# Performance work log

Hardware: AMD Instinct MI355X
Metric: run time of the kernel (lower is better)

The kernel has to match this reference:

```python
import jax, jax.numpy as jnp
import numpy as np

E = 512   # embed_dim
H = 16    # num_heads
D = E // H  # head_dim = 32
L = 2048  # target (query) length
S = 2048  # source (stored pattern) length
N = 4     # batch
LN_EPS = 1e-5


def setup_inputs() -> dict:
    key = jax.random.key(0)
    ks = jax.random.split(key, 8)
    inv_sqrt_e = 1.0 / np.sqrt(E).astype(np.float32)
    return {
        "query": jax.random.normal(ks[0], (L, N, E), jnp.float32),
        "key_in": jax.random.normal(ks[1], (S, N, E), jnp.float32),
        "value": jax.random.normal(ks[2], (S, N, E), jnp.float32),
        "scaling": jax.random.uniform(ks[3], (H,), jnp.float32),  # per-head beta
        "in_proj_weight": jax.random.normal(ks[4], (3 * E, E), jnp.float32) * inv_sqrt_e,
        "in_proj_bias": jnp.zeros((3 * E,), jnp.float32),
        "p_norm_weight": jnp.ones((D,), jnp.float32),
        "p_norm_bias": jnp.zeros((D,), jnp.float32),
        "out_proj_weight": jax.random.normal(ks[5], (E, E), jnp.float32) * inv_sqrt_e,
        "out_proj_bias": jnp.zeros((E,), jnp.float32),
    }


def reference(query, key_in, value, scaling, in_proj_weight, in_proj_bias,
              p_norm_weight, p_norm_bias, out_proj_weight, out_proj_bias):
    Lq, Nb, Ed = query.shape
    Sk = key_in.shape[0]
    # split packed in-projection (torch Linear convention: y = x @ W^T + b)
    wq, wk, wv = jnp.split(in_proj_weight, 3, axis=0)
    bq, bk, bv = jnp.split(in_proj_bias, 3, axis=0)
    q = jnp.einsum('lne,fe->lnf', query, wq) + bq
    k = jnp.einsum('sne,fe->snf', key_in, wk) + bk
    v = jnp.einsum('sne,fe->snf', value, wv) + bv
    # (len, N, H*D) -> (N, H, len, D)
    q = q.reshape(Lq, Nb, H, D).transpose(1, 2, 0, 3)
    k = k.reshape(Sk, Nb, H, D).transpose(1, 2, 0, 3)
    v = v.reshape(Sk, Nb, H, D).transpose(1, 2, 0, 3)

    def pattern_norm(x):
        # affine LayerNorm over the association (head) dimension D
        mu = jnp.mean(x, axis=-1, keepdims=True)
        var = jnp.mean(jnp.square(x - mu), axis=-1, keepdims=True)
        return (x - mu) * jax.lax.rsqrt(var + LN_EPS) * p_norm_weight + p_norm_bias

    k = pattern_norm(k)
    v = pattern_norm(v)

    beta = scaling.reshape(1, H, 1, 1)  # per-head inverse-temperature
    scores = jnp.einsum('nhld,nhsd->nhls', q * beta, k)  # [N,H,L,S]
    attn = jax.nn.softmax(scores, axis=-1)  # single Hopfield update (update_steps_max=0)
    out = jnp.einsum('nhls,nhsd->nhld', attn, v)  # [N,H,L,D]
    out = out.transpose(2, 0, 1, 3).reshape(Lq, Nb, H * D)
    out = jnp.einsum('lnf,of->lno', out, out_proj_weight) + out_proj_bias
    return out  # (L, N, E)
```

## Files before the change

kernel.cpp:

```cpp
#include <hip/hip_runtime.h>
#include <cstdint>

#define LN_EPS 1e-5f

typedef _Float16 f16;
typedef _Float16 half4_t __attribute__((ext_vector_type(4)));
typedef _Float16 half8_t __attribute__((ext_vector_type(8)));
typedef __fp16 fp16v2 __attribute__((ext_vector_type(2)));
typedef float f32x4 __attribute__((ext_vector_type(4)));

__device__ __forceinline__ void gl_lds16(const void* g, void* l) {
    __builtin_amdgcn_global_load_lds(
        (__attribute__((address_space(1))) void*)(uintptr_t)g,
        (__attribute__((address_space(3))) void*)(uint32_t)(uintptr_t)l,
        16, 0, 0);
}

__device__ __forceinline__ half4_t pack4(float a, float b, float c, float d) {
    fp16v2 lo = __builtin_amdgcn_cvt_pkrtz(a, b);
    fp16v2 hi = __builtin_amdgcn_cvt_pkrtz(c, d);
    half4_t r;
    r[0] = (f16)lo[0]; r[1] = (f16)lo[1]; r[2] = (f16)hi[0]; r[3] = (f16)hi[1];
    return r;
}

__global__ void k_cast(const float* __restrict__ W1f, const float* __restrict__ W2f,
                       const float* __restrict__ Xq, const float* __restrict__ Xk,
                       const float* __restrict__ Xv,
                       f16* __restrict__ W1h, f16* __restrict__ W2h,
                       f16* __restrict__ Xh) {
    int t = blockIdx.x * blockDim.x + threadIdx.x;
    const float4* src;
    half4_t* dst;
    int idx;
    if (t < 196608)      { src = (const float4*)W1f; dst = (half4_t*)W1h; idx = t; }
    else if (t < 262144) { src = (const float4*)W2f; dst = (half4_t*)W2h; idx = t - 196608; }
    else {
        int u = t - 262144;
        int s = u >> 20;
        idx = u & 1048575;
        src = (s == 0) ? (const float4*)Xq : ((s == 1) ? (const float4*)Xk : (const float4*)Xv);
        dst = (half4_t*)(Xh + (size_t)s * 4194304);
    }
    float4 v = src[idx];
    dst[idx] = pack4(v.x, v.y, v.z, v.w);
}

__global__ __launch_bounds__(256) void k_inproj(
    const f16* __restrict__ Xh, const f16* __restrict__ W1,
    const float* __restrict__ bias, const float* __restrict__ scaling,
    f16* __restrict__ Qg, f16* __restrict__ Kg, f16* __restrict__ Vg)
{
    __shared__ __align__(16) f16 Al[3][128 * 32];
    __shared__ __align__(16) f16 Bl[3][128 * 32];

    const int tid = threadIdx.x;
    const int m0 = blockIdx.x * 128;
    const int f0 = blockIdx.y * 128;
    const int sec = f0 >> 9;
    const f16* X = Xh + (size_t)sec * 4194304;
    f16* Ob = (sec == 0) ? Qg : ((sec == 1) ? Kg : Vg);

    const int wid = tid >> 6, ln = tid & 63, l15 = ln & 15, quad = ln >> 4;
    const int wm = wid >> 1, wn = wid & 1;
    const int srow = ln >> 2, sco = (ln & 3) * 8;

    f32x4 z4 = {0.f, 0.f, 0.f, 0.f};
    f32x4 acc[4][4];
    #pragma unroll
    for (int i = 0; i < 4; ++i)
        #pragma unroll
        for (int j = 0; j < 4; ++j) acc[i][j] = z4;

    auto issue = [&](int kt, int slot) {
        const int k0 = kt * 32;
        #pragma unroll
        for (int i = 0; i < 2; ++i) {
            int row = wid * 32 + i * 16 + srow;
            gl_lds16(W1 + (size_t)(f0 + row) * 512 + k0 + sco,
                     Bl[slot] + (wid * 32 + i * 16) * 32);
            gl_lds16(X + (size_t)(m0 + row) * 512 + k0 + sco,
                     Al[slot] + (wid * 32 + i * 16) * 32);
        }
    };
    issue(0, 0);
    issue(1, 1);

    int slot = 0;
    for (int kt = 0; kt < 16; ++kt) {
        if (kt < 15) asm volatile("s_waitcnt vmcnt(4)" ::: "memory");
        else         asm volatile("s_waitcnt vmcnt(0)" ::: "memory");
        __builtin_amdgcn_s_barrier();

        if (kt < 14) {
            int nb = slot + 2; if (nb >= 3) nb -= 3;
            issue(kt + 2, nb);
        }

        half8_t a[4], b[4];
        #pragma unroll
        for (int i = 0; i < 4; ++i)
            a[i] = *(const half8_t*)(Al[slot] + (wm * 64 + i * 16 + l15) * 32 + quad * 8);
        #pragma unroll
        for (int j = 0; j < 4; ++j)
            b[j] = *(const half8_t*)(Bl[slot] + (wn * 64 + j * 16 + l15) * 32 + quad * 8);
        __builtin_amdgcn_s_setprio(1);
        #pragma unroll
        for (int i = 0; i < 4; ++i)
            #pragma unroll
            for (int j = 0; j < 4; ++j)
                acc[i][j] = __builtin_amdgcn_mfma_f32_16x16x32_f16(b[j], a[i], acc[i][j], 0, 0, 0);
        __builtin_amdgcn_s_setprio(0);

        slot = slot + 1; if (slot == 3) slot = 0;
    }

    #pragma unroll
    for (int j = 0; j < 4; ++j) {
        int fb = f0 + wn * 64 + j * 16;
        int floc = (fb & 511) + quad * 4;
        int hh = floc >> 5;
        int cc = (floc >> 3) & 3, e0 = floc & 7;
        float sc2 = (sec == 0) ? scaling[hh] * 1.44269504f : 1.0f;
        float4 bs4 = *(const float4*)(bias + fb + quad * 4);
        #pragma unroll
        for (int i = 0; i < 4; ++i) {
            int rm = m0 + wm * 64 + i * 16 + l15;
            int l = rm >> 2, nb = rm & 3;
            int gg = nb * 16 + hh;
            *(half4_t*)(Ob + (size_t)gg * 65536 + (size_t)cc * 16384 + (size_t)l * 8 + e0) =
                pack4((acc[i][j][0] + bs4.x) * sc2, (acc[i][j][1] + bs4.y) * sc2,
                      (acc[i][j][2] + bs4.z) * sc2, (acc[i][j][3] + bs4.w) * sc2);
        }
    }
}

__global__ void k_norm_kv(f16* __restrict__ Kg, const f16* __restrict__ Vg,
                          const float* __restrict__ w, const float* __restrict__ b,
                          f16* __restrict__ Vtg) {
    __shared__ __align__(16) f16 T[32 * 64];
    const int t = threadIdx.x;
    const int seg = blockIdx.x, g = blockIdx.y;
    const int s_l = t >> 2, c = t & 3;
    const size_t base = (size_t)g * 65536 + (size_t)c * 16384 + (size_t)(seg * 64 + s_l) * 8;

    half8_t kv = *(const half8_t*)(Kg + base);
    half8_t vv = *(const half8_t*)(Vg + base);
    float kf[8], vf[8];
    float ks1 = 0.f, ks2 = 0.f, vs1 = 0.f, vs2 = 0.f;
    #pragma unroll
    for (int j = 0; j < 8; ++j) {
        kf[j] = (float)kv[j]; ks1 += kf[j]; ks2 += kf[j] * kf[j];
        vf[j] = (float)vv[j]; vs1 += vf[j]; vs2 += vf[j] * vf[j];
    }
    ks1 += __shfl_xor(ks1, 1); ks1 += __shfl_xor(ks1, 2);
    ks2 += __shfl_xor(ks2, 1); ks2 += __shfl_xor(ks2, 2);
    vs1 += __shfl_xor(vs1, 1); vs1 += __shfl_xor(vs1, 2);
    vs2 += __shfl_xor(vs2, 1); vs2 += __shfl_xor(vs2, 2);
    float kmu = ks1 * (1.f / 32.f), kvar = ks2 * (1.f / 32.f) - kmu * kmu;
    float vmu = vs1 * (1.f / 32.f), vvar = vs2 * (1.f / 32.f) - vmu * vmu;
    float krs = rsqrtf(kvar + LN_EPS), vrs = rsqrtf(vvar + LN_EPS);

    half8_t ky;
    int cs = s_l >> 3, es = s_l & 7;
    #pragma unroll
    for (int j = 0; j < 8; ++j) {
        int d = c * 8 + j;
        float wd = w[d], bd = b[d];
        ky[j] = (f16)((kf[j] - kmu) * krs * wd + bd);
        T[d * 64 + (cs ^ j) * 8 + es] = (f16)((vf[j] - vmu) * vrs * wd + bd);
    }
    *(half8_t*)(Kg + base) = ky;
    __syncthreads();
    int d_o = t >> 3, c_o = t & 7;
    half8_t out = *(const half8_t*)(T + d_o * 64 + c_o * 8);
    *(half8_t*)(Vtg + (size_t)(g * 32 + seg) * 2048 + d_o * 64 + c_o * 8) = out;
}

__global__ __launch_bounds__(256, 4) void k_flash(
    const f16* __restrict__ Qg, const f16* __restrict__ Kg,
    const f16* __restrict__ Vtg, f16* __restrict__ Og)
{
    __shared__ __align__(16) char smem[40960];

    const int tid = threadIdx.x, wid = tid >> 6, ln = tid & 63;
    const int l15 = ln & 15, quad = ln >> 4, l8 = ln & 7;
    char* Pw = smem + 24576 + wid * 4096;
    const int g = blockIdx.x, h = g & 15, n = g >> 4;
    const int q0 = blockIdx.y * 128;

    half8_t aq[2];
    #pragma unroll
    for (int i = 0; i < 2; ++i)
        aq[i] = *(const half8_t*)(Qg + (size_t)g * 65536 + (size_t)quad * 16384 +
                                  (size_t)(q0 + wid * 32 + i * 16 + l15) * 8);

    const f16* kp = Kg + (size_t)g * 65536 + (size_t)wid * 16384;
    const f16* vp = Vtg + (size_t)(g * 32) * 2048 + wid * 512;
    gl_lds16(kp + (size_t)ln * 8, smem + wid * 1024);
    gl_lds16(vp + (size_t)ln * 8, smem + 12288 + wid * 1024);
    gl_lds16(kp + 512 + (size_t)ln * 8, smem + 4096 + wid * 1024);
    gl_lds16(vp + 2048 + (size_t)ln * 8, smem + 12288 + 4096 + wid * 1024);
    kp += 1024;
    vp += 4096;

    half8_t onesf;
    {
        f16 o = (l15 == 0) ? (f16)1.0f : (f16)0.0f;
        #pragma unroll
        for (int j = 0; j < 8; ++j) onesf[j] = o;
    }

    f32x4 z4 = {0.f, 0.f, 0.f, 0.f};
    f32x4 accO[2][2], accSum[2];
    accO[0][0] = z4; accO[0][1] = z4; accO[1][0] = z4; accO[1][1] = z4;
    accSum[0] = z4; accSum[1] = z4;
    float m_i[2] = {-1e30f, -1e30f};

    int cur = 0;
    for (int st = 0; st < 32; ++st) {
        if (st < 31) asm volatile("s_waitcnt vmcnt(2)" ::: "memory");
        else         asm volatile("s_waitcnt vmcnt(0)" ::: "memory");
        __builtin_amdgcn_s_barrier();

        if (st < 30) {
            int nb = cur + 2; if (nb >= 3) nb -= 3;
            gl_lds16(kp + (size_t)ln * 8, smem + nb * 4096 + wid * 1024);
            gl_lds16(vp + (size_t)ln * 8, smem + 12288 + nb * 4096 + wid * 1024);
            kp += 512;
            vp += 2048;
        }
        const char* Kl = smem + cur * 4096;
        const char* Vt = smem + 12288 + cur * 4096;

        half8_t ak[4];
        #pragma unroll
        for (int mt = 0; mt < 4; ++mt)
            ak[mt] = *(const half8_t*)(Kl + quad * 1024 + (mt * 16 + l15) * 16);
        f32x4 accS[2][4];
        __builtin_amdgcn_s_setprio(1);
        #pragma unroll
        for (int i = 0; i < 2; ++i)
            #pragma unroll
            for (int mt = 0; mt < 4; ++mt)
                accS[i][mt] = __builtin_amdgcn_mfma_f32_16x16x32_f16(ak[mt], aq[i], z4, 0, 0, 0);
        __builtin_amdgcn_s_setprio(0);

        float mn[2];
        bool up = false;
        #pragma unroll
        for (int i = 0; i < 2; ++i) {
            float xm = fmaxf(fmaxf(accS[i][0][0], accS[i][0][1]),
                             fmaxf(accS[i][0][2], accS[i][0][3]));
            #pragma unroll
            for (int mt = 1; mt < 4; ++mt)
                xm = fmaxf(xm, fmaxf(fmaxf(accS[i][mt][0], accS[i][mt][1]),
                                     fmaxf(accS[i][mt][2], accS[i][mt][3])));
            xm = fmaxf(xm, __shfl_xor(xm, 16));
            xm = fmaxf(xm, __shfl_xor(xm, 32));
            up = up || (xm > m_i[i] + 8.f);
            mn[i] = fmaxf(m_i[i], xm);
        }
        if (__ballot(up)) {
            #pragma unroll
            for (int i = 0; i < 2; ++i) {
                float alpha = __builtin_amdgcn_exp2f(m_i[i] - mn[i]);
                #pragma unroll
                for (int dt = 0; dt < 2; ++dt)
                    #pragma unroll
                    for (int r = 0; r < 4; ++r) accO[i][dt][r] *= alpha;
                #pragma unroll
                for (int r = 0; r < 4; ++r) accSum[i][r] *= alpha;
                m_i[i] = mn[i];
            }
        }

        #pragma unroll
        for (int i = 0; i < 2; ++i) {
            #pragma unroll
            for (int mt = 0; mt < 4; ++mt) {
                float p0 = __builtin_amdgcn_exp2f(accS[i][mt][0] - m_i[i]);
                float p1 = __builtin_amdgcn_exp2f(accS[i][mt][1] - m_i[i]);
                float p2 = __builtin_amdgcn_exp2f(accS[i][mt][2] - m_i[i]);
                float p3 = __builtin_amdgcn_exp2f(accS[i][mt][3] - m_i[i]);
                int ch = (mt * 2 + (quad >> 1)) ^ l8;
                *(half4_t*)(Pw + (i * 16 + l15) * 128 + ch * 16 + (quad & 1) * 8) =
                    pack4(p0, p1, p2, p3);
            }
        }

        #pragma unroll
        for (int kt = 0; kt < 2; ++kt) {
            half8_t av[2], bp[2];
            #pragma unroll
            for (int dt = 0; dt < 2; ++dt) {
                int d = dt * 16 + l15;
                int cp = (kt * 4 + quad) ^ (l15 & 7);
                av[dt] = *(const half8_t*)(Vt + d * 128 + cp * 16);
            }
            #pragma unroll
            for (int i = 0; i < 2; ++i)
                bp[i] = *(const half8_t*)(Pw + (i * 16 + l15) * 128 +
                                          (((kt * 4 + quad) ^ l8) * 16));
            __builtin_amdgcn_s_setprio(1);
            #pragma unroll
            for (int i = 0; i < 2; ++i) {
                #pragma unroll
                for (int dt = 0; dt < 2; ++dt)
                    accO[i][dt] = __builtin_amdgcn_mfma_f32_16x16x32_f16(av[dt], bp[i], accO[i][dt], 0, 0, 0);
                accSum[i] = __builtin_amdgcn_mfma_f32_16x16x32_f16(onesf, bp[i], accSum[i], 0, 0, 0);
            }
            __builtin_amdgcn_s_setprio(0);
        }

        cur = cur + 1; if (cur == 3) cur = 0;
    }

    #pragma unroll
    for (int i = 0; i < 2; ++i) {
        float li = __shfl(accSum[i][0], l15);
        float inv = 1.f / li;
        #pragma unroll
        for (int dt = 0; dt < 2; ++dt)
            *(half4_t*)(Pw + (i * 16 + l15) * 80 + (dt * 16 + quad * 4) * 2) =
                pack4(accO[i][dt][0] * inv, accO[i][dt][1] * inv,
                      accO[i][dt][2] * inv, accO[i][dt][3] * inv);
    }
    int q2 = ln >> 1, hf = ln & 1;
    half8_t o0 = *(const half8_t*)(Pw + q2 * 80 + hf * 32);
    half8_t o1 = *(const half8_t*)(Pw + q2 * 80 + hf * 32 + 16);
    size_t rowe = ((size_t)(n * 2048 + q0 + wid * 32 + q2)) * 512 + h * 32 + hf * 16;
    *(half8_t*)(Og + rowe) = o0;
    *(half8_t*)(Og + rowe + 8) = o1;
}

__global__ __launch_bounds__(256) void k_outproj(
    const f16* __restrict__ A, const f16* __restrict__ W2,
    const float* __restrict__ bias, float* __restrict__ Out)
{
    __shared__ __align__(16) f16 Al[3][64 * 32];
    __shared__ __align__(16) f16 Bl[3][128 * 32];

    const int tid = threadIdx.x;
    const int m0 = blockIdx.x * 64;
    const int f0 = blockIdx.y * 128;
    const int wid = tid >> 6, ln = tid & 63, l15 = ln & 15, quad = ln >> 4;
    const int wm = wid >> 1, wn = wid & 1;
    const int srow = ln >> 2, sco = (ln & 3) * 8;

    f32x4 z4 = {0.f, 0.f, 0.f, 0.f};
    f32x4 acc[2][4];
    #pragma unroll
    for (int i = 0; i < 2; ++i)
        #pragma unroll
        for (int j = 0; j < 4; ++j) acc[i][j] = z4;

    auto issue = [&](int kt, int slot) {
        const int k0 = kt * 32;
        int arow = wid * 16 + srow;
        gl_lds16(A + (size_t)(m0 + arow) * 512 + k0 + sco,
                 Al[slot] + wid * 512);
        #pragma unroll
        for (int i = 0; i < 2; ++i) {
            int brow = wid * 32 + i * 16 + srow;
            gl_lds16(W2 + (size_t)(f0 + brow) * 512 + k0 + sco,
                     Bl[slot] + (wid * 32 + i * 16) * 32);
        }
    };
    issue(0, 0);
    issue(1, 1);

    int slot = 0;
    for (int kt = 0; kt < 16; ++kt) {
        if (kt < 15) asm volatile("s_waitcnt vmcnt(3)" ::: "memory");
        else         asm volatile("s_waitcnt vmcnt(0)" ::: "memory");
        __builtin_amdgcn_s_barrier();

        if (kt < 14) {
            int nb = slot + 2; if (nb >= 3) nb -= 3;
            issue(kt + 2, nb);
        }

        half8_t a[2], b[4];
        #pragma unroll
        for (int i = 0; i < 2; ++i)
            a[i] = *(const half8_t*)(Al[slot] + (wm * 32 + i * 16 + l15) * 32 + quad * 8);
        #pragma unroll
        for (int j = 0; j < 4; ++j)
            b[j] = *(const half8_t*)(Bl[slot] + (wn * 64 + j * 16 + l15) * 32 + quad * 8);
        __builtin_amdgcn_s_setprio(1);
        #pragma unroll
        for (int i = 0; i < 2; ++i)
            #pragma unroll
            for (int j = 0; j < 4; ++j)
                acc[i][j] = __builtin_amdgcn_mfma_f32_16x16x32_f16(b[j], a[i], acc[i][j], 0, 0, 0);
        __builtin_amdgcn_s_setprio(0);

        slot = slot + 1; if (slot == 3) slot = 0;
    }

    #pragma unroll
    for (int j = 0; j < 4; ++j) {
        int fb = f0 + wn * 64 + j * 16;
        float4 bs4 = *(const float4*)(bias + fb + quad * 4);
        #pragma unroll
        for (int i = 0; i < 2; ++i) {
            int rm = m0 + wm * 32 + i * 16 + l15;
            int orow = (rm & 2047) * 4 + (rm >> 11);
            float4 o;
            o.x = acc[i][j][0] + bs4.x;
            o.y = acc[i][j][1] + bs4.y;
            o.z = acc[i][j][2] + bs4.z;
            o.w = acc[i][j][3] + bs4.w;
            *(float4*)(Out + (size_t)orow * 512 + fb + quad * 4) = o;
        }
    }
}

extern "C" void kernel_launch(void* const* d_in, const int* in_sizes, int n_in,
                              void* d_out, int out_size, void* d_ws, size_t ws_size,
                              hipStream_t stream) {
    const float* query   = (const float*)d_in[0];
    const float* key_in  = (const float*)d_in[1];
    const float* value   = (const float*)d_in[2];
    const float* scaling = (const float*)d_in[3];
    const float* ipw     = (const float*)d_in[4];
    const float* ipb     = (const float*)d_in[5];
    const float* pnw     = (const float*)d_in[6];
    const float* pnb     = (const float*)d_in[7];
    const float* opw     = (const float*)d_in[8];
    const float* opb     = (const float*)d_in[9];
    float* out = (float*)d_out;

    f16* Qg  = (f16*)d_ws;
    f16* Kg  = Qg + (size_t)4194304;
    f16* Vg  = Qg + (size_t)8388608;
    f16* W1  = Qg + (size_t)12582912;
    f16* W2  = Qg + (size_t)13369344;
    f16* Xh  = Qg + (size_t)13631488;
    f16* Vtg = Xh;
    f16* Og  = Vg;

    k_cast<<<13312, 256, 0, stream>>>(ipw, opw, query, key_in, value, W1, W2, Xh);
    k_inproj<<<dim3(64, 12), 256, 0, stream>>>(Xh, W1, ipb, scaling, Qg, Kg, Vg);
    k_norm_kv<<<dim3(32, 64), 256, 0, stream>>>(Kg, Vg, pnw, pnb, Vtg);
    k_flash<<<dim3(64, 16), 256, 0, stream>>>(Qg, Kg, Vtg, Og);
    k_outproj<<<dim3(128, 4), 256, 0, stream>>>(Og, W2, opb, out);
}
```

Measured before the change: 213.0 us.

## Stage GEMM epilogues through LDS for coalesced stores; grid-stride cast kernel

The in-projection and out-projection epilogues now write their accumulator tiles into a reused shared-memory pool, using an XOR swizzle in the in-projection, before streaming them to global memory in wide contiguous chunks. The previous direct stores were scattered 8-byte or row-strided 16-byte writes. The cast kernel now runs a quarter of the blocks, each thread converting four elements. The extra LDS round trip and barriers add latency in exchange for better write coalescing.

```diff
diff --git a/kernel.cpp b/kernel.cpp
--- a/kernel.cpp
+++ b/kernel.cpp
@@ -29,21 +29,25 @@
                        const float* __restrict__ Xv,
                        f16* __restrict__ W1h, f16* __restrict__ W2h,
                        f16* __restrict__ Xh) {
-    int t = blockIdx.x * blockDim.x + threadIdx.x;
-    const float4* src;
-    half4_t* dst;
-    int idx;
-    if (t < 196608)      { src = (const float4*)W1f; dst = (half4_t*)W1h; idx = t; }
-    else if (t < 262144) { src = (const float4*)W2f; dst = (half4_t*)W2h; idx = t - 196608; }
-    else {
-        int u = t - 262144;
-        int s = u >> 20;
-        idx = u & 1048575;
-        src = (s == 0) ? (const float4*)Xq : ((s == 1) ? (const float4*)Xk : (const float4*)Xv);
-        dst = (half4_t*)(Xh + (size_t)s * 4194304);
-    }
-    float4 v = src[idx];
-    dst[idx] = pack4(v.x, v.y, v.z, v.w);
+    int t0 = blockIdx.x * blockDim.x + threadIdx.x;
+    #pragma unroll
+    for (int rep = 0; rep < 4; ++rep) {
+        int t = t0 + rep * 851968;
+        const float4* src;
+        half4_t* dst;
+        int idx;
+        if (t < 196608)      { src = (const float4*)W1f; dst = (half4_t*)W1h; idx = t; }
+        else if (t < 262144) { src = (const float4*)W2f; dst = (half4_t*)W2h; idx = t - 196608; }
+        else {
+            int u = t - 262144;
+            int s = u >> 20;
+            idx = u & 1048575;
+            src = (s == 0) ? (const float4*)Xq : ((s == 1) ? (const float4*)Xk : (const float4*)Xv);
+            dst = (half4_t*)(Xh + (size_t)s * 4194304);
+        }
+        float4 v = src[idx];
+        dst[idx] = pack4(v.x, v.y, v.z, v.w);
+    }
 }
 
 __global__ __launch_bounds__(256) void k_inproj(
@@ -51,8 +55,7 @@
     const float* __restrict__ bias, const float* __restrict__ scaling,
     f16* __restrict__ Qg, f16* __restrict__ Kg, f16* __restrict__ Vg)
 {
-    __shared__ __align__(16) f16 Al[3][128 * 32];
-    __shared__ __align__(16) f16 Bl[3][128 * 32];
+    __shared__ __align__(16) char pool[49152];
 
     const int tid = threadIdx.x;
     const int m0 = blockIdx.x * 128;
@@ -74,13 +77,15 @@
 
     auto issue = [&](int kt, int slot) {
         const int k0 = kt * 32;
+        f16* As = (f16*)(pool + slot * 16384);
+        f16* Bs = (f16*)(pool + slot * 16384 + 8192);
         #pragma unroll
         for (int i = 0; i < 2; ++i) {
             int row = wid * 32 + i * 16 + srow;
             gl_lds16(W1 + (size_t)(f0 + row) * 512 + k0 + sco,
-                     Bl[slot] + (wid * 32 + i * 16) * 32);
+                     Bs + (wid * 32 + i * 16) * 32);
             gl_lds16(X + (size_t)(m0 + row) * 512 + k0 + sco,
-                     Al[slot] + (wid * 32 + i * 16) * 32);
+                     As + (wid * 32 + i * 16) * 32);
         }
     };
     issue(0, 0);
@@ -97,13 +102,15 @@
             issue(kt + 2, nb);
         }
 
+        const f16* As = (const f16*)(pool + slot * 16384);
+        const f16* Bs = (const f16*)(pool + slot * 16384 + 8192);
         half8_t a[4], b[4];
         #pragma unroll
         for (int i = 0; i < 4; ++i)
-            a[i] = *(const half8_t*)(Al[slot] + (wm * 64 + i * 16 + l15) * 32 + quad * 8);
+            a[i] = *(const half8_t*)(As + (wm * 64 + i * 16 + l15) * 32 + quad * 8);
         #pragma unroll
         for (int j = 0; j < 4; ++j)
-            b[j] = *(const half8_t*)(Bl[slot] + (wn * 64 + j * 16 + l15) * 32 + quad * 8);
+            b[j] = *(const half8_t*)(Bs + (wn * 64 + j * 16 + l15) * 32 + quad * 8);
         __builtin_amdgcn_s_setprio(1);
         #pragma unroll
         for (int i = 0; i < 4; ++i)
@@ -115,22 +122,40 @@
         slot = slot + 1; if (slot == 3) slot = 0;
     }
 
+    __syncthreads();
+    f16* Ep = (f16*)pool;
+
     #pragma unroll
     for (int j = 0; j < 4; ++j) {
-        int fb = f0 + wn * 64 + j * 16;
-        int floc = (fb & 511) + quad * 4;
-        int hh = floc >> 5;
-        int cc = (floc >> 3) & 3, e0 = floc & 7;
+        int floc0 = wn * 64 + j * 16 + quad * 4;
+        int fb = f0 + floc0;
+        int hh = (fb & 511) >> 5;
         float sc2 = (sec == 0) ? scaling[hh] * 1.44269504f : 1.0f;
-        float4 bs4 = *(const float4*)(bias + fb + quad * 4);
+        float4 bs4 = *(const float4*)(bias + fb);
         #pragma unroll
         for (int i = 0; i < 4; ++i) {
-            int rm = m0 + wm * 64 + i * 16 + l15;
-            int l = rm >> 2, nb = rm & 3;
-            int gg = nb * 16 + hh;
-            *(half4_t*)(Ob + (size_t)gg * 65536 + (size_t)cc * 16384 + (size_t)l * 8 + e0) =
+            int mloc = wm * 64 + i * 16 + l15;
+            int key = (mloc >> 2) & 7;
+            *(half4_t*)(Ep + mloc * 128 + (floc0 ^ (key << 3))) =
                 pack4((acc[i][j][0] + bs4.x) * sc2, (acc[i][j][1] + bs4.y) * sc2,
                       (acc[i][j][2] + bs4.z) * sc2, (acc[i][j][3] + bs4.w) * sc2);
+        }
+    }
+    __syncthreads();
+
+    {
+        int fgrp = (tid >> 6) * 4 + quad;
+        int fs = (f0 & 511) + fgrp * 8;
+        int hh = fs >> 5, cc = (fs >> 3) & 3;
+        #pragma unroll
+        for (int it = 0; it < 8; ++it) {
+            int nb = it & 3, lblk = it >> 2;
+            int L = lblk * 16 + l15;
+            int mloc = nb + 4 * L;
+            half8_t v = *(const half8_t*)(Ep + mloc * 128 + ((fgrp ^ (L & 7)) << 3));
+            int gg = nb * 16 + hh;
+            size_t l = (size_t)(m0 >> 2) + L;
+            *(half8_t*)(Ob + (size_t)gg * 65536 + (size_t)cc * 16384 + l * 8) = v;
         }
     }
 }
@@ -338,8 +363,7 @@
     const f16* __restrict__ A, const f16* __restrict__ W2,
     const float* __restrict__ bias, float* __restrict__ Out)
 {
-    __shared__ __align__(16) f16 Al[3][64 * 32];
-    __shared__ __align__(16) f16 Bl[3][128 * 32];
+    __shared__ __align__(16) char pool[36864];
 
     const int tid = threadIdx.x;
     const int m0 = blockIdx.x * 64;
@@ -357,14 +381,16 @@
 
     auto issue = [&](int kt, int slot) {
         const int k0 = kt * 32;
+        f16* As = (f16*)(pool + slot * 12288);
+        f16* Bs = (f16*)(pool + slot * 12288 + 4096);
         int arow = wid * 16 + srow;
         gl_lds16(A + (size_t)(m0 + arow) * 512 + k0 + sco,
-                 Al[slot] + wid * 512);
+                 As + wid * 512);
         #pragma unroll
         for (int i = 0; i < 2; ++i) {
             int brow = wid * 32 + i * 16 + srow;
             gl_lds16(W2 + (size_t)(f0 + brow) * 512 + k0 + sco,
-                     Bl[slot] + (wid * 32 + i * 16) * 32);
+                     Bs + (wid * 32 + i * 16) * 32);
         }
     };
     issue(0, 0);
@@ -381,13 +407,15 @@
             issue(kt + 2, nb);
         }
 
+        const f16* As = (const f16*)(pool + slot * 12288);
+        const f16* Bs = (const f16*)(pool + slot * 12288 + 4096);
         half8_t a[2], b[4];
         #pragma unroll
         for (int i = 0; i < 2; ++i)
-            a[i] = *(const half8_t*)(Al[slot] + (wm * 32 + i * 16 + l15) * 32 + quad * 8);
+            a[i] = *(const half8_t*)(As + (wm * 32 + i * 16 + l15) * 32 + quad * 8);
         #pragma unroll
         for (int j = 0; j < 4; ++j)
-            b[j] = *(const half8_t*)(Bl[slot] + (wn * 64 + j * 16 + l15) * 32 + quad * 8);
+            b[j] = *(const half8_t*)(Bs + (wn * 64 + j * 16 + l15) * 32 + quad * 8);
         __builtin_amdgcn_s_setprio(1);
         #pragma unroll
         for (int i = 0; i < 2; ++i)
@@ -399,20 +427,35 @@
         slot = slot + 1; if (slot == 3) slot = 0;
     }
 
+    __syncthreads();
+    float* Ef = (float*)pool;
+
     #pragma unroll
     for (int j = 0; j < 4; ++j) {
-        int fb = f0 + wn * 64 + j * 16;
-        float4 bs4 = *(const float4*)(bias + fb + quad * 4);
+        int floc0 = wn * 64 + j * 16 + quad * 4;
+        float4 bs4 = *(const float4*)(bias + f0 + floc0);
         #pragma unroll
         for (int i = 0; i < 2; ++i) {
-            int rm = m0 + wm * 32 + i * 16 + l15;
-            int orow = (rm & 2047) * 4 + (rm >> 11);
+            int mloc = wm * 32 + i * 16 + l15;
             float4 o;
             o.x = acc[i][j][0] + bs4.x;
             o.y = acc[i][j][1] + bs4.y;
             o.z = acc[i][j][2] + bs4.z;
             o.w = acc[i][j][3] + bs4.w;
-            *(float4*)(Out + (size_t)orow * 512 + fb + quad * 4) = o;
+            *(float4*)(Ef + mloc * 132 + floc0) = o;
+        }
+    }
+    __syncthreads();
+
+    {
+        int hw = tid >> 5, lane32 = tid & 31;
+        #pragma unroll
+        for (int it = 0; it < 8; ++it) {
+            int row = it * 8 + hw;
+            float4 v = *(const float4*)(Ef + row * 132 + lane32 * 4);
+            int rm = m0 + row;
+            int orow = (rm & 2047) * 4 + (rm >> 11);
+            *(float4*)(Out + (size_t)orow * 512 + f0 + lane32 * 4) = v;
         }
     }
 }
@@ -441,7 +484,7 @@
     f16* Vtg = Xh;
     f16* Og  = Vg;
 
-    k_cast<<<13312, 256, 0, stream>>>(ipw, opw, query, key_in, value, W1, W2, Xh);
+    k_cast<<<3328, 256, 0, stream>>>(ipw, opw, query, key_in, value, W1, W2, Xh);
     k_inproj<<<dim3(64, 12), 256, 0, stream>>>(Xh, W1, ipb, scaling, Qg, Kg, Vg);
     k_norm_kv<<<dim3(32, 64), 256, 0, stream>>>(Kg, Vg, pnw, pnb, Vtg);
     k_flash<<<dim3(64, 16), 256, 0, stream>>>(Qg, Kg, Vtg, Og);
```

Result: no change. 210.5 us (-1.1%).
